# Kernel optimization log

Hardware: AMD Instinct MI355X
Metric: run time of the kernel (lower is better)

## Reference

```python
import jax, jax.numpy as jnp
import numpy as np

P, E, D = 128, 32, 64          # n_proxy_sets, n_elements, d
B, SEG_LEN = 1024, 128          # number of segments, per-segment length
N = B * SEG_LEN                 # total elements


def setup_inputs() -> dict:
    key = jax.random.key(0)
    k_x, k_p = jax.random.split(key)
    x = jax.random.normal(k_x, (N, D), dtype=jnp.float32)
    proxy_sets = jax.random.normal(k_p, (P, E, D), dtype=jnp.float32)
    index = jnp.full((B,), SEG_LEN, dtype=jnp.int32)  # segment lengths, sum == N
    return {"x": x, "proxy_sets": proxy_sets, "index": index}


def reference(x, proxy_sets, index):
    # sim_mat[p,e,n] = proxy_sets[p,e,:] . x[n,:]
    sim = jnp.einsum("ped,nd->pen", proxy_sets, x)     # [P,E,N]
    t = jnp.max(sim, axis=1)                             # [P,N]  max over proxy elements
    # ragged segment sum over N driven by segment lengths `index`
    seg_ids = jnp.repeat(jnp.arange(B, dtype=jnp.int32), index,
                         total_repeat_length=N)          # [N]
    pooled = jax.ops.segment_sum(t.T, seg_ids, num_segments=B)  # [B,P]
    pooled = pooled.astype(jnp.float32)
    # F.normalize(p=2, dim=1): divide by max(||.||_2, eps)
    norm = jnp.linalg.norm(pooled, axis=1, keepdims=True)
    return pooled / jnp.maximum(norm, 1e-12)
```

## Files before the change

### kernel.cpp

```cpp
#include <hip/hip_runtime.h>
#include <hip/hip_bf16.h>
#include <stdint.h>


typedef short short8 __attribute__((ext_vector_type(8)));
typedef __bf16 bf16x8 __attribute__((ext_vector_type(8)));
typedef float floatx16 __attribute__((ext_vector_type(16)));

#define NPROXY 128
#define NELEM  32
#define DIM    64
#define NSEG   1024
#define PROXY_ELEMS (NPROXY * NELEM * DIM)

__device__ __forceinline__ unsigned short f32_to_bf16_rne(float f) {
  union { float f; unsigned int u; } v; v.f = f;
  unsigned int r = v.u + 0x7fffu + ((v.u >> 16) & 1u);
  return (unsigned short)(r >> 16);
}

__global__ void sc_prep(const float* __restrict__ proxy,
                        const int* __restrict__ index,
                        short* __restrict__ pb,
                        int* __restrict__ offs,
                        float* __restrict__ out) {
  const int bx = blockIdx.x, t = threadIdx.x;
  if (bx == 0) {
    __shared__ int lsum[256];
    const int base = t * 4;
    const int i0 = index[base + 0], i1 = index[base + 1];
    const int i2 = index[base + 2], i3 = index[base + 3];
    const int s = i0 + i1 + i2 + i3;
    lsum[t] = s;
    __syncthreads();
    for (int off = 1; off < 256; off <<= 1) {
      int v = (t >= off) ? lsum[t - off] : 0;
      __syncthreads();
      lsum[t] += v;
      __syncthreads();
    }
    const int ex = lsum[t] - s;
    offs[base + 0] = ex;
    offs[base + 1] = ex + i0;
    offs[base + 2] = ex + i0 + i1;
    offs[base + 3] = ex + i0 + i1 + i2;
    if (t == 255) offs[NSEG] = ex + s;
  } else {
    const int idx = ((bx - 1) * 256 + t) * 4;
    float4 v = *(const float4*)(proxy + idx);
    ushort4 o;
    o.x = f32_to_bf16_rne(v.x); o.y = f32_to_bf16_rne(v.y);
    o.z = f32_to_bf16_rne(v.z); o.w = f32_to_bf16_rne(v.w);
    *(ushort4*)(pb + idx) = o;
    if (bx <= 128) {
      const int oidx = ((bx - 1) * 256 + t) * 4;
      *(float4*)(out + oidx) = make_float4(0.f, 0.f, 0.f, 0.f);
    }
  }
}

__global__ __launch_bounds__(256, 2) void sc_main(
    const float* __restrict__ x,
    const short* __restrict__ pb,
    const int* __restrict__ offs,
    float* __restrict__ out) {
  const int b = blockIdx.x;
  const int tid = threadIdx.x;
  const int lane = tid & 63;
  const int w = tid >> 6;
  const int l31 = lane & 31;
  const int h = lane >> 5;

  const int start = offs[b];
  const int len = offs[b + 1] - start;
  const int nchunks = (len + 127) >> 7;
  const bool single_chunk = (nchunks == 1);

  const short* pbase = pb + l31 * DIM + h * 8;

  for (int c = 0; c < nchunks; ++c) {
    const int c0 = c << 7;

    short8 bfrag[4][4];
#pragma unroll
    for (int t4 = 0; t4 < 4; ++t4) {
      const int nl = c0 + t4 * 32 + l31;
      const bool valid = (nl < len);
      const float* xr = x + (size_t)(start + nl) * DIM + h * 8;
#pragma unroll
      for (int kk = 0; kk < 4; ++kk) {
        float4 f0 = make_float4(0.f, 0.f, 0.f, 0.f), f1 = f0;
        if (valid) {
          f0 = *(const float4*)(xr + kk * 16);
          f1 = *(const float4*)(xr + kk * 16 + 4);
        }
        short8 fr;
        fr[0] = (short)f32_to_bf16_rne(f0.x);
        fr[1] = (short)f32_to_bf16_rne(f0.y);
        fr[2] = (short)f32_to_bf16_rne(f0.z);
        fr[3] = (short)f32_to_bf16_rne(f0.w);
        fr[4] = (short)f32_to_bf16_rne(f1.x);
        fr[5] = (short)f32_to_bf16_rne(f1.y);
        fr[6] = (short)f32_to_bf16_rne(f1.z);
        fr[7] = (short)f32_to_bf16_rne(f1.w);
        bfrag[t4][kk] = fr;
      }
    }

    auto process_p = [&](int p, short8 (&acur)[4], short8 (&anxt)[4], bool pf) {
      if (pf) {
        const short* ap = pbase + (size_t)(p + 4) * (NELEM * DIM);
#pragma unroll
        for (int kk = 0; kk < 4; ++kk)
          anxt[kk] = *(const short8*)(ap + kk * 16);
      }
      floatx16 acc0, acc1, acc2, acc3;
#pragma unroll
      for (int r = 0; r < 16; ++r) {
        acc0[r] = 0.f; acc1[r] = 0.f; acc2[r] = 0.f; acc3[r] = 0.f;
      }
#pragma unroll
      for (int kk = 0; kk < 4; ++kk) {
        bf16x8 a = __builtin_bit_cast(bf16x8, acur[kk]);
        acc0 = __builtin_amdgcn_mfma_f32_32x32x16_bf16(
            a, __builtin_bit_cast(bf16x8, bfrag[0][kk]), acc0, 0, 0, 0);
        acc1 = __builtin_amdgcn_mfma_f32_32x32x16_bf16(
            a, __builtin_bit_cast(bf16x8, bfrag[1][kk]), acc1, 0, 0, 0);
        acc2 = __builtin_amdgcn_mfma_f32_32x32x16_bf16(
            a, __builtin_bit_cast(bf16x8, bfrag[2][kk]), acc2, 0, 0, 0);
        acc3 = __builtin_amdgcn_mfma_f32_32x32x16_bf16(
            a, __builtin_bit_cast(bf16x8, bfrag[3][kk]), acc3, 0, 0, 0);
      }
      float m0 = acc0[0], m1 = acc1[0], m2 = acc2[0], m3 = acc3[0];
#pragma unroll
      for (int r = 1; r < 16; ++r) {
        m0 = fmaxf(m0, acc0[r]); m1 = fmaxf(m1, acc1[r]);
        m2 = fmaxf(m2, acc2[r]); m3 = fmaxf(m3, acc3[r]);
      }
      m0 = fmaxf(m0, __shfl_xor(m0, 32, 64));
      m1 = fmaxf(m1, __shfl_xor(m1, 32, 64));
      m2 = fmaxf(m2, __shfl_xor(m2, 32, 64));
      m3 = fmaxf(m3, __shfl_xor(m3, 32, 64));
      float s = (m0 + m1) + (m2 + m3);
#pragma unroll
      for (int off = 1; off <= 16; off <<= 1) s += __shfl_xor(s, off, 64);
      if (lane == 0) {
        float* dst = out + (b << 7) + p;
        if (single_chunk) *dst = s;
        else atomicAdd(dst, s);
      }
    };

    short8 afA[4], afB[4];
    {
      const short* ap = pbase + (size_t)w * (NELEM * DIM);
#pragma unroll
      for (int kk = 0; kk < 4; ++kk)
        afA[kk] = *(const short8*)(ap + kk * 16);
    }
    for (int i = 0; i < 32; i += 2) {
      process_p(w + 4 * i, afA, afB, true);
      process_p(w + 4 * (i + 1), afB, afA, i < 30);
    }
  }
}

__global__ void sc_norm(float* __restrict__ out) {
  const int b = blockIdx.x;
  const int t = threadIdx.x;
  const float v = out[(b << 7) + t];
  float sq = v * v;
#pragma unroll
  for (int off = 1; off <= 32; off <<= 1) sq += __shfl_xor(sq, off, 64);
  __shared__ float wsum[2];
  if ((t & 63) == 0) wsum[t >> 6] = sq;
  __syncthreads();
  const float denom = fmaxf(sqrtf(wsum[0] + wsum[1]), 1e-12f);
  out[(b << 7) + t] = v / denom;
}

extern "C" void kernel_launch(void* const* d_in, const int* in_sizes, int n_in,
                              void* d_out, int out_size, void* d_ws, size_t ws_size,
                              hipStream_t stream) {
  (void)in_sizes; (void)n_in; (void)out_size; (void)ws_size;
  const float* x = (const float*)d_in[0];
  const float* proxy = (const float*)d_in[1];
  const int* index = (const int*)d_in[2];
  float* out = (float*)d_out;

  int* offs = (int*)d_ws;
  short* pb = (short*)((char*)d_ws + 8192);

  sc_prep<<<257, 256, 0, stream>>>(proxy, index, pb, offs, out);
  sc_main<<<NSEG, 256, 0, stream>>>(x, pb, offs, out);
  sc_norm<<<NSEG, 128, 0, stream>>>(out);
}
```

Baseline: 150.1 us.

## Fuse normalization into main kernel and split waves across proxies and rows

Each block now owns its whole segment. Per-proxy partial sums are kept in shared memory instead of going through global atomics, and the L2 normalization is done in-kernel, so the separate norm kernel and the zeroing of the output are gone. Waves are re-partitioned: each wave covers 64 proxies by 64 rows, which halves the x fragments held in registers. Launch bounds are raised to 4 blocks per SM. The cost is that each wave now loads proxy fragments for 64 proxies per chunk and a ~35KB shared buffer is added, which may limit occupancy.

```diff
diff --git a/kernel.cpp b/kernel.cpp
--- a/kernel.cpp
+++ b/kernel.cpp
@@ -1,5 +1,4 @@
 #include <hip/hip_runtime.h>
-#include <hip/hip_bf16.h>
 #include <stdint.h>
 
 
@@ -7,11 +6,11 @@
 typedef __bf16 bf16x8 __attribute__((ext_vector_type(8)));
 typedef float floatx16 __attribute__((ext_vector_type(16)));
 
-#define NPROXY 128
-#define NELEM  32
-#define DIM    64
-#define NSEG   1024
-#define PROXY_ELEMS (NPROXY * NELEM * DIM)
+#define NELEM 32
+#define DIM   64
+#define NSEG  1024
+#define PSTRIDE (NELEM * DIM)
+#define LROW 68
 
 __device__ __forceinline__ unsigned short f32_to_bf16_rne(float f) {
   union { float f; unsigned int u; } v; v.f = f;
@@ -22,8 +21,7 @@
 __global__ void sc_prep(const float* __restrict__ proxy,
                         const int* __restrict__ index,
                         short* __restrict__ pb,
-                        int* __restrict__ offs,
-                        float* __restrict__ out) {
+                        int* __restrict__ offs) {
   const int bx = blockIdx.x, t = threadIdx.x;
   if (bx == 0) {
     __shared__ int lsum[256];
@@ -52,39 +50,55 @@
     o.x = f32_to_bf16_rne(v.x); o.y = f32_to_bf16_rne(v.y);
     o.z = f32_to_bf16_rne(v.z); o.w = f32_to_bf16_rne(v.w);
     *(ushort4*)(pb + idx) = o;
-    if (bx <= 128) {
-      const int oidx = ((bx - 1) * 256 + t) * 4;
-      *(float4*)(out + oidx) = make_float4(0.f, 0.f, 0.f, 0.f);
-    }
   }
 }
 
-__global__ __launch_bounds__(256, 2) void sc_main(
+__device__ __forceinline__ float max16(const floatx16& a) {
+  float r0 = fmaxf(fmaxf(a[0], a[1]), a[2]);
+  float r1 = fmaxf(fmaxf(a[3], a[4]), a[5]);
+  float r2 = fmaxf(fmaxf(a[6], a[7]), a[8]);
+  float r3 = fmaxf(fmaxf(a[9], a[10]), a[11]);
+  float r4 = fmaxf(fmaxf(a[12], a[13]), a[14]);
+  float r5 = fmaxf(fmaxf(r0, r1), r2);
+  float r6 = fmaxf(fmaxf(r3, r4), a[15]);
+  return fmaxf(r5, r6);
+}
+
+__global__ __launch_bounds__(256, 4) void sc_main(
     const float* __restrict__ x,
     const short* __restrict__ pb,
     const int* __restrict__ offs,
     float* __restrict__ out) {
+  __shared__ float buf[128 * LROW];
+  __shared__ float red[4];
+
   const int b = blockIdx.x;
   const int tid = threadIdx.x;
   const int lane = tid & 63;
   const int w = tid >> 6;
+  const int wn = w & 1;
+  const int wp = w >> 1;
   const int l31 = lane & 31;
   const int h = lane >> 5;
 
   const int start = offs[b];
   const int len = offs[b + 1] - start;
-  const int nchunks = (len + 127) >> 7;
-  const bool single_chunk = (nchunks == 1);
-
-  const short* pbase = pb + l31 * DIM + h * 8;
+  int nchunks = (len + 127) >> 7;
+  if (nchunks < 1) nchunks = 1;
+
+  floatx16 zc;
+#pragma unroll
+  for (int r = 0; r < 16; ++r) zc[r] = 0.f;
+
+  const short* abase = pb + (size_t)(wp * 64) * PSTRIDE + l31 * DIM + h * 8;
 
   for (int c = 0; c < nchunks; ++c) {
     const int c0 = c << 7;
 
-    short8 bfrag[4][4];
-#pragma unroll
-    for (int t4 = 0; t4 < 4; ++t4) {
-      const int nl = c0 + t4 * 32 + l31;
+    short8 bfrag[2][4];
+#pragma unroll
+    for (int t4 = 0; t4 < 2; ++t4) {
+      const int nl = c0 + wn * 64 + t4 * 32 + l31;
       const bool valid = (nl < len);
       const float* xr = x + (size_t)(start + nl) * DIM + h * 8;
 #pragma unroll
@@ -107,76 +121,75 @@
       }
     }
 
-    auto process_p = [&](int p, short8 (&acur)[4], short8 (&anxt)[4], bool pf) {
+    auto process = [&](int i, short8 (&cur)[4], short8 (&nxt)[4], bool pf) {
       if (pf) {
-        const short* ap = pbase + (size_t)(p + 4) * (NELEM * DIM);
+        const short* ap = abase + (size_t)(i + 1) * PSTRIDE;
 #pragma unroll
         for (int kk = 0; kk < 4; ++kk)
-          anxt[kk] = *(const short8*)(ap + kk * 16);
-      }
-      floatx16 acc0, acc1, acc2, acc3;
-#pragma unroll
-      for (int r = 0; r < 16; ++r) {
-        acc0[r] = 0.f; acc1[r] = 0.f; acc2[r] = 0.f; acc3[r] = 0.f;
-      }
+          nxt[kk] = *(const short8*)(ap + kk * 16);
+      }
+      floatx16 a0, a1;
 #pragma unroll
       for (int kk = 0; kk < 4; ++kk) {
-        bf16x8 a = __builtin_bit_cast(bf16x8, acur[kk]);
-        acc0 = __builtin_amdgcn_mfma_f32_32x32x16_bf16(
-            a, __builtin_bit_cast(bf16x8, bfrag[0][kk]), acc0, 0, 0, 0);
-        acc1 = __builtin_amdgcn_mfma_f32_32x32x16_bf16(
-            a, __builtin_bit_cast(bf16x8, bfrag[1][kk]), acc1, 0, 0, 0);
-        acc2 = __builtin_amdgcn_mfma_f32_32x32x16_bf16(
-            a, __builtin_bit_cast(bf16x8, bfrag[2][kk]), acc2, 0, 0, 0);
-        acc3 = __builtin_amdgcn_mfma_f32_32x32x16_bf16(
-            a, __builtin_bit_cast(bf16x8, bfrag[3][kk]), acc3, 0, 0, 0);
-      }
-      float m0 = acc0[0], m1 = acc1[0], m2 = acc2[0], m3 = acc3[0];
-#pragma unroll
-      for (int r = 1; r < 16; ++r) {
-        m0 = fmaxf(m0, acc0[r]); m1 = fmaxf(m1, acc1[r]);
-        m2 = fmaxf(m2, acc2[r]); m3 = fmaxf(m3, acc3[r]);
-      }
+        bf16x8 a = __builtin_bit_cast(bf16x8, cur[kk]);
+        bf16x8 b0 = __builtin_bit_cast(bf16x8, bfrag[0][kk]);
+        bf16x8 b1 = __builtin_bit_cast(bf16x8, bfrag[1][kk]);
+        if (kk == 0) {
+          a0 = __builtin_amdgcn_mfma_f32_32x32x16_bf16(a, b0, zc, 0, 0, 0);
+          a1 = __builtin_amdgcn_mfma_f32_32x32x16_bf16(a, b1, zc, 0, 0, 0);
+        } else {
+          a0 = __builtin_amdgcn_mfma_f32_32x32x16_bf16(a, b0, a0, 0, 0, 0);
+          a1 = __builtin_amdgcn_mfma_f32_32x32x16_bf16(a, b1, a1, 0, 0, 0);
+        }
+      }
+      float m0 = max16(a0);
+      float m1 = max16(a1);
       m0 = fmaxf(m0, __shfl_xor(m0, 32, 64));
       m1 = fmaxf(m1, __shfl_xor(m1, 32, 64));
-      m2 = fmaxf(m2, __shfl_xor(m2, 32, 64));
-      m3 = fmaxf(m3, __shfl_xor(m3, 32, 64));
-      float s = (m0 + m1) + (m2 + m3);
-#pragma unroll
-      for (int off = 1; off <= 16; off <<= 1) s += __shfl_xor(s, off, 64);
-      if (lane == 0) {
-        float* dst = out + (b << 7) + p;
-        if (single_chunk) *dst = s;
-        else atomicAdd(dst, s);
+      const float s = m0 + m1;
+      const int p = wp * 64 + i;
+      const int idx = p * LROW + wn * 32 + l31;
+      if (h == 0) {
+        float prev = (c == 0) ? 0.f : buf[idx];
+        buf[idx] = prev + s;
       }
     };
 
     short8 afA[4], afB[4];
-    {
-      const short* ap = pbase + (size_t)w * (NELEM * DIM);
-#pragma unroll
-      for (int kk = 0; kk < 4; ++kk)
-        afA[kk] = *(const short8*)(ap + kk * 16);
-    }
-    for (int i = 0; i < 32; i += 2) {
-      process_p(w + 4 * i, afA, afB, true);
-      process_p(w + 4 * (i + 1), afB, afA, i < 30);
+#pragma unroll
+    for (int kk = 0; kk < 4; ++kk)
+      afA[kk] = *(const short8*)(abase + kk * 16);
+    for (int i = 0; i < 64; i += 2) {
+      process(i, afA, afB, true);
+      process(i + 1, afB, afA, i < 62);
     }
   }
-}
-
-__global__ void sc_norm(float* __restrict__ out) {
-  const int b = blockIdx.x;
-  const int t = threadIdx.x;
-  const float v = out[(b << 7) + t];
-  float sq = v * v;
+  __syncthreads();
+
+  const int p2 = tid >> 1, part = tid & 1;
+  const float* bp = buf + p2 * LROW + part * 32;
+  float4 v0 = *(const float4*)(bp + 0);
+  float4 v1 = *(const float4*)(bp + 4);
+  float4 v2 = *(const float4*)(bp + 8);
+  float4 v3 = *(const float4*)(bp + 12);
+  float4 v4 = *(const float4*)(bp + 16);
+  float4 v5 = *(const float4*)(bp + 20);
+  float4 v6 = *(const float4*)(bp + 24);
+  float4 v7 = *(const float4*)(bp + 28);
+  float s32 = ((v0.x + v0.y) + (v0.z + v0.w)) + ((v1.x + v1.y) + (v1.z + v1.w)) +
+              ((v2.x + v2.y) + (v2.z + v2.w)) + ((v3.x + v3.y) + (v3.z + v3.w)) +
+              ((v4.x + v4.y) + (v4.z + v4.w)) + ((v5.x + v5.y) + (v5.z + v5.w)) +
+              ((v6.x + v6.y) + (v6.z + v6.w)) + ((v7.x + v7.y) + (v7.z + v7.w));
+  const float s64 = s32 + __shfl_xor(s32, 1, 64);
+
+  float sq = part ? 0.f : s64 * s64;
 #pragma unroll
   for (int off = 1; off <= 32; off <<= 1) sq += __shfl_xor(sq, off, 64);
-  __shared__ float wsum[2];
-  if ((t & 63) == 0) wsum[t >> 6] = sq;
+  if (lane == 0) red[w] = sq;
   __syncthreads();
-  const float denom = fmaxf(sqrtf(wsum[0] + wsum[1]), 1e-12f);
-  out[(b << 7) + t] = v / denom;
+  const float ss = (red[0] + red[1]) + (red[2] + red[3]);
+  const float inv = 1.f / fmaxf(sqrtf(ss), 1e-12f);
+  if (part == 0) out[(b << 7) + p2] = s64 * inv;
 }
 
 extern "C" void kernel_launch(void* const* d_in, const int* in_sizes, int n_in,
@@ -191,7 +204,6 @@
   int* offs = (int*)d_ws;
   short* pb = (short*)((char*)d_ws + 8192);
 
-  sc_prep<<<257, 256, 0, stream>>>(proxy, index, pb, offs, out);
+  sc_prep<<<257, 256, 0, stream>>>(proxy, index, pb, offs);
   sc_main<<<NSEG, 256, 0, stream>>>(x, pb, offs, out);
-  sc_norm<<<NSEG, 128, 0, stream>>>(out);
-}
+}
```

Measured after the change: 193.8 us. 29.1% more time.
